# Performance work log

Hardware: AMD Instinct MI355X
Metric: run time of the kernel (lower is better)

The kernel has to match this reference:

```python
import jax, jax.numpy as jnp
import numpy as np

B, N, D, H = 1, 2048, 2048, 16
K = D // H  # head dim = 128


def setup_inputs() -> dict:
    key = jax.random.key(0)
    k1, k2, k3 = jax.random.split(key, 3)
    x = jax.random.normal(k1, (B, N, D), dtype=jnp.float32)
    # torch Linear(D, 3D, bias=False): y = x @ W.T; we store the transposed weight directly.
    W_qkv = jax.random.normal(k2, (D, 3 * D), dtype=jnp.float32) * 0.02
    W_out = jax.random.normal(k3, (D, D), dtype=jnp.float32) * 0.02
    return {"x": x, "W_qkv": W_qkv, "W_out": W_out}


def reference(x, W_qkv, W_out):
    b, n, d = x.shape
    qkv = (x @ W_qkv).reshape(b, n, 3, H, K)  # [B,N,3,H,K]
    q, k, v = qkv[:, :, 0], qkv[:, :, 1], qkv[:, :, 2]  # each [B,N,H,K]
    scale = np.float32(1.0 / np.sqrt(K))
    scores = jnp.einsum('bnhk,bmhk->bnhm', q, k) * scale  # [B,N,H,M]
    causal_mask = jnp.tril(jnp.ones((n, n), dtype=bool))  # [N,M]
    scores = jnp.where(causal_mask[None, :, None, :], scores, jnp.float32(-jnp.inf))
    probs = jax.nn.softmax(scores, axis=-1)
    attn = jnp.einsum('bnhm,bmhk->bnhk', probs, v).reshape(b, n, d)
    return attn @ W_out
```

## Files before the change

### kernel.cpp

```cpp
#include <hip/hip_runtime.h>
#include <hip/hip_bf16.h>
#include <math.h>

#define N_SEQ  2048
#define DMODEL 2048
#define NHEAD  16
#define HDIM   128
#define QKV_LD 6144

typedef __attribute__((ext_vector_type(8))) short bf16x8;
typedef __attribute__((ext_vector_type(4))) float f32x4;

__device__ __forceinline__ ushort f2bf(float x) {
    union { float f; unsigned u; } v; v.f = x;
    unsigned r = (v.u + 0x7fffu + ((v.u >> 16) & 1u)) >> 16;
    return (ushort)r;
}
__device__ __forceinline__ float bf2f(ushort h) {
    union { unsigned u; float f; } v; v.u = ((unsigned)h) << 16;
    return v.f;
}

__global__ __launch_bounds__(256)
void convert_split(const float* __restrict__ in, ushort* __restrict__ oh,
                   ushort* __restrict__ ol, int n4)
{
    int i = blockIdx.x * 256 + threadIdx.x;
    if (i >= n4) return;
    float4 v = ((const float4*)in)[i];
    ushort4 h, l;
    h.x = f2bf(v.x); l.x = f2bf(v.x - bf2f(h.x));
    h.y = f2bf(v.y); l.y = f2bf(v.y - bf2f(h.y));
    h.z = f2bf(v.z); l.z = f2bf(v.z - bf2f(h.z));
    h.w = f2bf(v.w); l.w = f2bf(v.w - bf2f(h.w));
    ((ushort4*)oh)[i] = h;
    ((ushort4*)ol)[i] = l;
}

__global__ __launch_bounds__(256)
void convert_split_t(const float* __restrict__ in, ushort* __restrict__ oh,
                     ushort* __restrict__ ol, int R, int C)
{
    __shared__ float T[64][65];
    const int t = threadIdx.x;
    const int c0 = blockIdx.x * 64, r0 = blockIdx.y * 64;
    #pragma unroll
    for (int p = 0; p < 4; ++p) {
        int r = (t >> 4) + p * 16;
        int c4 = (t & 15) * 4;
        float4 v = *(const float4*)&in[(size_t)(r0 + r) * C + c0 + c4];
        T[r][c4] = v.x; T[r][c4 + 1] = v.y; T[r][c4 + 2] = v.z; T[r][c4 + 3] = v.w;
    }
    __syncthreads();
    #pragma unroll
    for (int p = 0; p < 4; ++p) {
        int c = (t >> 4) + p * 16;
        int r4 = (t & 15) * 4;
        float f0 = T[r4][c], f1 = T[r4 + 1][c], f2 = T[r4 + 2][c], f3 = T[r4 + 3][c];
        ushort4 h, l;
        h.x = f2bf(f0); l.x = f2bf(f0 - bf2f(h.x));
        h.y = f2bf(f1); l.y = f2bf(f1 - bf2f(h.y));
        h.z = f2bf(f2); l.z = f2bf(f2 - bf2f(h.z));
        h.w = f2bf(f3); l.w = f2bf(f3 - bf2f(h.w));
        *(ushort4*)&oh[(size_t)(c0 + c) * R + r0 + r4] = h;
        *(ushort4*)&ol[(size_t)(c0 + c) * R + r0 + r4] = l;
    }
}

__global__ __launch_bounds__(256)
void transpose_v(const ushort* __restrict__ qkvh, ushort* __restrict__ vt)
{
    __shared__ ushort T[64][72];
    const int t = threadIdx.x;
    const int c0 = blockIdx.x * 64, n0 = blockIdx.y * 64;
    #pragma unroll
    for (int p = 0; p < 2; ++p) {
        int r = (t >> 3) + p * 32;
        int u = (t & 7) * 8;
        *(bf16x8*)&T[r][u] = *(const bf16x8*)&qkvh[(size_t)(n0 + r) * QKV_LD + 2 * DMODEL + c0 + u];
    }
    __syncthreads();
    #pragma unroll
    for (int p = 0; p < 2; ++p) {
        int d = (t >> 3) + p * 32;
        int ju = (t & 7) * 8;
        bf16x8 o;
        #pragma unroll
        for (int i = 0; i < 8; ++i) o[i] = (short)T[ju + i][d];
        *(bf16x8*)&vt[(size_t)(c0 + d) * N_SEQ + n0 + ju] = o;
    }
}

#define GBM 256
#define GBN 256
#define GBK 32
#define GPITCH 68

template<bool BF16OUT>
__global__ __launch_bounds__(512, 2)
void gemm_bf16x3_v2(const ushort* __restrict__ Ah_g, const ushort* __restrict__ Al_g,
                    const ushort* __restrict__ Bh_g, const ushort* __restrict__ Bl_g,
                    ushort* __restrict__ Ch, ushort* __restrict__ Cl,
                    float* __restrict__ Cf, int M, int N, int K)
{
    __shared__ ushort bufA[2][GBM * GPITCH];
    __shared__ ushort bufB[2][GBN * GPITCH];

    const int t = threadIdx.x;
    const int l = t & 63;
    const int w = t >> 6;
    const int l15 = l & 15, kgr = l >> 4;
    const int wm = (w >> 2) * 128;
    const int wn = (w & 3) * 64;

    const int nbx = N / GBN, nby = M / GBM;
    const int nwg = nbx * nby;
    int flat = blockIdx.x + blockIdx.y * nbx;
    if ((nwg & 7) == 0) flat = (flat & 7) * (nwg >> 3) + (flat >> 3);
    const int bm = (flat / nbx) * GBM;
    const int bn = (flat % nbx) * GBN;

    const int rA = t >> 1;
    const int hA = t & 1;
    const ushort* gA = (hA ? Al_g : Ah_g) + (size_t)(bm + rA) * K;
    const ushort* gB = (hA ? Bl_g : Bh_g) + (size_t)(bn + rA) * K;

    bf16x8 stA[4], stB[4];
    auto load_regs = [&](int k0) {
        #pragma unroll
        for (int j = 0; j < 4; ++j) {
            stA[j] = *(const bf16x8*)(gA + k0 + j * 8);
            stB[j] = *(const bf16x8*)(gB + k0 + j * 8);
        }
    };
    auto write_lds = [&](int b) {
        #pragma unroll
        for (int j = 0; j < 4; ++j) {
            *(bf16x8*)&bufA[b][rA * GPITCH + hA * 32 + j * 8] = stA[j];
            *(bf16x8*)&bufB[b][rA * GPITCH + hA * 32 + j * 8] = stB[j];
        }
    };

    f32x4 acc[8][4] = {};

    const int nt = K / GBK;
    load_regs(0);
    write_lds(0);
    load_regs(GBK);

    for (int i = 0; i < nt; ++i) {
        const int c = i & 1;
        asm volatile("s_waitcnt lgkmcnt(0)\n\ts_barrier" ::: "memory");
        if (i + 1 < nt) write_lds(c ^ 1);
        if (i + 2 < nt) load_regs((i + 2) * GBK);

        bf16x8 bh[4], bl[4];
        #pragma unroll
        for (int nf = 0; nf < 4; ++nf) {
            const int r = wn + nf * 16 + l15;
            bh[nf] = *(const bf16x8*)&bufB[c][r * GPITCH + kgr * 8];
            bl[nf] = *(const bf16x8*)&bufB[c][r * GPITCH + 32 + kgr * 8];
        }
        #pragma unroll
        for (int mf = 0; mf < 8; ++mf) {
            const int r = wm + mf * 16 + l15;
            bf16x8 ah = *(const bf16x8*)&bufA[c][r * GPITCH + kgr * 8];
            bf16x8 al = *(const bf16x8*)&bufA[c][r * GPITCH + 32 + kgr * 8];
            #pragma unroll
            for (int nf = 0; nf < 4; ++nf) {
                acc[mf][nf] = __builtin_amdgcn_mfma_f32_16x16x32_bf16(ah, bh[nf], acc[mf][nf], 0, 0, 0);
                acc[mf][nf] = __builtin_amdgcn_mfma_f32_16x16x32_bf16(ah, bl[nf], acc[mf][nf], 0, 0, 0);
                acc[mf][nf] = __builtin_amdgcn_mfma_f32_16x16x32_bf16(al, bh[nf], acc[mf][nf], 0, 0, 0);
            }
        }
    }

    #pragma unroll
    for (int mf = 0; mf < 8; ++mf)
        #pragma unroll
        for (int nf = 0; nf < 4; ++nf)
            #pragma unroll
            for (int r = 0; r < 4; ++r) {
                const int m = bm + wm + mf * 16 + kgr * 4 + r;
                const int n = bn + wn + nf * 16 + l15;
                const float v = acc[mf][nf][r];
                if constexpr (BF16OUT) {
                    ushort h = f2bf(v);
                    Ch[(size_t)m * N + n] = h;
                    Cl[(size_t)m * N + n] = f2bf(v - bf2f(h));
                } else {
                    Cf[(size_t)m * N + n] = v;
                }
            }
}

template<bool BF16OUT>
__global__ __launch_bounds__(256, 2)
void gemm_bf16x3(const ushort* __restrict__ Ah_g, const ushort* __restrict__ Al_g,
                 const ushort* __restrict__ Bh_g, const ushort* __restrict__ Bl_g,
                 ushort* __restrict__ Ch, ushort* __restrict__ Cl,
                 float* __restrict__ Cf, int M, int N, int K)
{
    __shared__ ushort Ah[128 * 40], Al[128 * 40], Bh[128 * 40], Bl[128 * 40];
    const int t = threadIdx.x;
    const int l = t & 63;
    const int w = t >> 6;
    const int l15 = l & 15, kgr = l >> 4;
    const int wm = (w >> 1) * 64, wn = (w & 1) * 64;
    const int bm = blockIdx.y * 128, bn = blockIdx.x * 128;
    const int sr = t >> 2, sku = (t & 3) * 8;

    f32x4 acc[4][4] = {};
    bf16x8 sA[4], sB[4];

    auto load_stage = [&](int k0) {
        const size_t a0 = (size_t)(bm + sr) * K + k0 + sku;
        const size_t a1 = (size_t)(bm + sr + 64) * K + k0 + sku;
        sA[0] = *(const bf16x8*)(Ah_g + a0);
        sA[1] = *(const bf16x8*)(Ah_g + a1);
        sA[2] = *(const bf16x8*)(Al_g + a0);
        sA[3] = *(const bf16x8*)(Al_g + a1);
        const size_t b0 = (size_t)(bn + sr) * K + k0 + sku;
        const size_t b1 = (size_t)(bn + sr + 64) * K + k0 + sku;
        sB[0] = *(const bf16x8*)(Bh_g + b0);
        sB[1] = *(const bf16x8*)(Bh_g + b1);
        sB[2] = *(const bf16x8*)(Bl_g + b0);
        sB[3] = *(const bf16x8*)(Bl_g + b1);
    };
    auto write_stage = [&]() {
        *(bf16x8*)&Ah[sr * 40 + sku]        = sA[0];
        *(bf16x8*)&Ah[(sr + 64) * 40 + sku] = sA[1];
        *(bf16x8*)&Al[sr * 40 + sku]        = sA[2];
        *(bf16x8*)&Al[(sr + 64) * 40 + sku] = sA[3];
        *(bf16x8*)&Bh[sr * 40 + sku]        = sB[0];
        *(bf16x8*)&Bh[(sr + 64) * 40 + sku] = sB[1];
        *(bf16x8*)&Bl[sr * 40 + sku]        = sB[2];
        *(bf16x8*)&Bl[(sr + 64) * 40 + sku] = sB[3];
    };

    load_stage(0);
    for (int k0 = 0; k0 < K; k0 += 32) {
        __syncthreads();
        write_stage();
        __syncthreads();
        if (k0 + 32 < K) load_stage(k0 + 32);

        bf16x8 ah[4], al[4], bh[4], bl[4];
        #pragma unroll
        for (int mf = 0; mf < 4; ++mf) {
            ah[mf] = *(const bf16x8*)&Ah[(wm + mf * 16 + l15) * 40 + kgr * 8];
            al[mf] = *(const bf16x8*)&Al[(wm + mf * 16 + l15) * 40 + kgr * 8];
        }
        #pragma unroll
        for (int nf = 0; nf < 4; ++nf) {
            bh[nf] = *(const bf16x8*)&Bh[(wn + nf * 16 + l15) * 40 + kgr * 8];
            bl[nf] = *(const bf16x8*)&Bl[(wn + nf * 16 + l15) * 40 + kgr * 8];
        }
        #pragma unroll
        for (int mf = 0; mf < 4; ++mf)
            #pragma unroll
            for (int nf = 0; nf < 4; ++nf) {
                acc[mf][nf] = __builtin_amdgcn_mfma_f32_16x16x32_bf16(ah[mf], bh[nf], acc[mf][nf], 0, 0, 0);
                acc[mf][nf] = __builtin_amdgcn_mfma_f32_16x16x32_bf16(ah[mf], bl[nf], acc[mf][nf], 0, 0, 0);
                acc[mf][nf] = __builtin_amdgcn_mfma_f32_16x16x32_bf16(al[mf], bh[nf], acc[mf][nf], 0, 0, 0);
            }
    }

    #pragma unroll
    for (int mf = 0; mf < 4; ++mf)
        #pragma unroll
        for (int nf = 0; nf < 4; ++nf)
            #pragma unroll
            for (int r = 0; r < 4; ++r) {
                const int m = bm + wm + mf * 16 + kgr * 4 + r;
                const int n = bn + wn + nf * 16 + l15;
                const float v = acc[mf][nf][r];
                if constexpr (BF16OUT) {
                    ushort h = f2bf(v);
                    Ch[(size_t)m * N + n] = h;
                    Cl[(size_t)m * N + n] = f2bf(v - bf2f(h));
                } else {
                    Cf[(size_t)m * N + n] = v;
                }
            }
}

__global__ __launch_bounds__(256, 2)
void attn_mfma(const ushort* __restrict__ qkvh, const ushort* __restrict__ qkvl,
               const ushort* __restrict__ vt,
               ushort* __restrict__ oh, ushort* __restrict__ ol)
{
    __shared__ ushort Kh[64 * 136], Kl[64 * 136], Vts[128 * 72], St[4 * 16 * 72];
    const int t = threadIdx.x;
    const int l = t & 63;
    const int w = t >> 6;
    const int l15 = l & 15, kgr = l >> 4;
    const int h = blockIdx.y, qb = blockIdx.x;
    const int q0 = qb * 64 + w * 16;

    bf16x8 qh[4], ql[4];
    {
        const size_t base = (size_t)(q0 + l15) * QKV_LD + h * HDIM;
        #pragma unroll
        for (int kc = 0; kc < 4; ++kc) {
            qh[kc] = *(const bf16x8*)(qkvh + base + kc * 32 + kgr * 8);
            ql[kc] = *(const bf16x8*)(qkvl + base + kc * 32 + kgr * 8);
        }
    }

    f32x4 o[8] = {};
    float m_run[4], l_run[4];
    #pragma unroll
    for (int r = 0; r < 4; ++r) { m_run[r] = -1e30f; l_run[r] = 0.f; }

    bf16x8 sKh[4], sKl[4], sV[4];
    auto load_tile = [&](int jb) {
        #pragma unroll
        for (int i = 0; i < 4; ++i) {
            int r = (t >> 4) + i * 16;
            size_t g = (size_t)(jb + r) * QKV_LD + DMODEL + h * HDIM + (t & 15) * 8;
            sKh[i] = *(const bf16x8*)(qkvh + g);
            sKl[i] = *(const bf16x8*)(qkvl + g);
        }
        #pragma unroll
        for (int i = 0; i < 4; ++i) {
            int d = (t >> 3) + i * 32;
            sV[i] = *(const bf16x8*)(vt + (size_t)(h * HDIM + d) * N_SEQ + jb + (t & 7) * 8);
        }
    };
    auto write_tile = [&]() {
        #pragma unroll
        for (int i = 0; i < 4; ++i) {
            int r = (t >> 4) + i * 16;
            *(bf16x8*)&Kh[r * 136 + (t & 15) * 8] = sKh[i];
            *(bf16x8*)&Kl[r * 136 + (t & 15) * 8] = sKl[i];
        }
        #pragma unroll
        for (int i = 0; i < 4; ++i) {
            int d = (t >> 3) + i * 32;
            *(bf16x8*)&Vts[d * 72 + (t & 7) * 8] = sV[i];
        }
    };

    const float scale = 0.08838834764831845f;

    load_tile(0);
    for (int jt = 0; jt <= qb; ++jt) {
        const int jb = jt * 64;
        __syncthreads();
        write_tile();
        __syncthreads();
        if (jt < qb) load_tile(jb + 64);

        float sv[4][4];
        #pragma unroll
        for (int jf = 0; jf < 4; ++jf) {
            f32x4 sacc = {};
            #pragma unroll
            for (int kc = 0; kc < 4; ++kc) {
                bf16x8 kh = *(const bf16x8*)&Kh[(jf * 16 + l15) * 136 + kc * 32 + kgr * 8];
                bf16x8 kl = *(const bf16x8*)&Kl[(jf * 16 + l15) * 136 + kc * 32 + kgr * 8];
                sacc = __builtin_amdgcn_mfma_f32_16x16x32_bf16(qh[kc], kh, sacc, 0, 0, 0);
                sacc = __builtin_amdgcn_mfma_f32_16x16x32_bf16(qh[kc], kl, sacc, 0, 0, 0);
                sacc = __builtin_amdgcn_mfma_f32_16x16x32_bf16(ql[kc], kh, sacc, 0, 0, 0);
            }
            const int j = jb + jf * 16 + l15;
            #pragma unroll
            for (int r = 0; r < 4; ++r) {
                const int q = q0 + kgr * 4 + r;
                sv[jf][r] = (j > q) ? -1e30f : sacc[r] * scale;
            }
        }

        float corr[4], p[4][4];
        #pragma unroll
        for (int r = 0; r < 4; ++r) {
            float tm = fmaxf(fmaxf(sv[0][r], sv[1][r]), fmaxf(sv[2][r], sv[3][r]));
            tm = fmaxf(tm, __shfl_xor(tm, 1));
            tm = fmaxf(tm, __shfl_xor(tm, 2));
            tm = fmaxf(tm, __shfl_xor(tm, 4));
            tm = fmaxf(tm, __shfl_xor(tm, 8));
            const float nm = fmaxf(m_run[r], tm);
            corr[r] = __expf(m_run[r] - nm);
            m_run[r] = nm;
            float rs = 0.f;
            #pragma unroll
            for (int jf = 0; jf < 4; ++jf) { p[jf][r] = __expf(sv[jf][r] - nm); rs += p[jf][r]; }
            rs += __shfl_xor(rs, 1);
            rs += __shfl_xor(rs, 2);
            rs += __shfl_xor(rs, 4);
            rs += __shfl_xor(rs, 8);
            l_run[r] = l_run[r] * corr[r] + rs;
        }

        #pragma unroll
        for (int jf = 0; jf < 4; ++jf)
            #pragma unroll
            for (int r = 0; r < 4; ++r)
                St[w * 1152 + (kgr * 4 + r) * 72 + jf * 16 + l15] = f2bf(p[jf][r]);

        #pragma unroll
        for (int df = 0; df < 8; ++df)
            #pragma unroll
            for (int r = 0; r < 4; ++r) o[df][r] *= corr[r];

        #pragma unroll
        for (int jc = 0; jc < 2; ++jc) {
            bf16x8 pa = *(const bf16x8*)&St[w * 1152 + l15 * 72 + jc * 32 + kgr * 8];
            #pragma unroll
            for (int df = 0; df < 8; ++df) {
                bf16x8 vb = *(const bf16x8*)&Vts[(df * 16 + l15) * 72 + jc * 32 + kgr * 8];
                o[df] = __builtin_amdgcn_mfma_f32_16x16x32_bf16(pa, vb, o[df], 0, 0, 0);
            }
        }
    }

    #pragma unroll
    for (int r = 0; r < 4; ++r) l_run[r] = 1.f / l_run[r];
    #pragma unroll
    for (int df = 0; df < 8; ++df)
        #pragma unroll
        for (int r = 0; r < 4; ++r) {
            const float v = o[df][r] * l_run[r];
            const size_t a = (size_t)(q0 + kgr * 4 + r) * DMODEL + h * HDIM + df * 16 + l15;
            const ushort hh = f2bf(v);
            oh[a] = hh;
            ol[a] = f2bf(v - bf2f(hh));
        }
}

extern "C" void kernel_launch(void* const* d_in, const int* in_sizes, int n_in,
                              void* d_out, int out_size, void* d_ws, size_t ws_size,
                              hipStream_t stream)
{
    const float* x    = (const float*)d_in[0];
    const float* Wqkv = (const float*)d_in[1];
    const float* Wout = (const float*)d_in[2];
    float* outp = (float*)d_out;

    const size_t O_XHI = 0;
    const size_t O_XLO = 8388608;
    const size_t O_WT  = 16777216;
    const size_t O_QKV = 67108864;

    char* ws = (char*)d_ws;
    ushort* x_hi   = (ushort*)(ws + O_XHI);
    ushort* x_lo   = (ushort*)(ws + O_XLO);
    ushort* wqt_hi = (ushort*)(ws + O_WT);
    ushort* wqt_lo = (ushort*)(ws + O_WT + 25165824);
    ushort* qkv_hi = (ushort*)(ws + O_QKV);
    ushort* qkv_lo = (ushort*)(ws + O_QKV + 25165824);
    ushort* wot_hi = (ushort*)(ws + O_WT);
    ushort* wot_lo = (ushort*)(ws + O_WT + 8388608);
    ushort* vt     = (ushort*)(ws + O_WT + 16777216);
    ushort* at_hi  = (ushort*)(ws + O_XHI);
    ushort* at_lo  = (ushort*)(ws + O_XLO);

    convert_split<<<dim3(N_SEQ * DMODEL / 4 / 256), 256, 0, stream>>>(
        x, x_hi, x_lo, N_SEQ * DMODEL / 4);
    convert_split_t<<<dim3(QKV_LD / 64, DMODEL / 64), 256, 0, stream>>>(
        Wqkv, wqt_hi, wqt_lo, DMODEL, QKV_LD);
    gemm_bf16x3_v2<true><<<dim3(QKV_LD / GBN, N_SEQ / GBM), 512, 0, stream>>>(
        x_hi, x_lo, wqt_hi, wqt_lo, qkv_hi, qkv_lo, nullptr,
        N_SEQ, QKV_LD, DMODEL);
    convert_split_t<<<dim3(DMODEL / 64, DMODEL / 64), 256, 0, stream>>>(
        Wout, wot_hi, wot_lo, DMODEL, DMODEL);
    transpose_v<<<dim3(DMODEL / 64, N_SEQ / 64), 256, 0, stream>>>(qkv_hi, vt);
    attn_mfma<<<dim3(N_SEQ / 64, NHEAD), 256, 0, stream>>>(
        qkv_hi, qkv_lo, vt, at_hi, at_lo);
    gemm_bf16x3<false><<<dim3(DMODEL / 128, N_SEQ / 128), 256, 0, stream>>>(
        at_hi, at_lo, wot_hi, wot_lo, nullptr, nullptr, outp,
        N_SEQ, DMODEL, DMODEL);
}
```

Measured before the change: 519.3 us.

## Shrink QKV GEMM tile, pair causal query blocks in attention, unify GEMMs

The QKV projection GEMM moves from 256x256 tiles with 512 threads to 128x128 tiles with 256 threads, giving more workgroups across the CUs. The same double-buffered kernel now also handles the output projection, replacing the older single-buffered GEMM. Attention gives each workgroup two query blocks, b and 31-b, so the causal work per block is even. It also double-buffers the K/V tiles with lighter barriers. The cost is more registers for the two sets of Q fragments and accumulators, which may lower occupancy.

```diff
diff --git a/kernel.cpp b/kernel.cpp
--- a/kernel.cpp
+++ b/kernel.cpp
@@ -91,34 +91,27 @@
     }
 }
 
-#define GBM 256
-#define GBN 256
-#define GBK 32
-#define GPITCH 68
-
 template<bool BF16OUT>
-__global__ __launch_bounds__(512, 2)
-void gemm_bf16x3_v2(const ushort* __restrict__ Ah_g, const ushort* __restrict__ Al_g,
+__global__ __launch_bounds__(256, 2)
+void gemm_bf16x3_v3(const ushort* __restrict__ Ah_g, const ushort* __restrict__ Al_g,
                     const ushort* __restrict__ Bh_g, const ushort* __restrict__ Bl_g,
                     ushort* __restrict__ Ch, ushort* __restrict__ Cl,
                     float* __restrict__ Cf, int M, int N, int K)
 {
-    __shared__ ushort bufA[2][GBM * GPITCH];
-    __shared__ ushort bufB[2][GBN * GPITCH];
+    __shared__ ushort bufA[2][128 * 68];
+    __shared__ ushort bufB[2][128 * 68];
 
     const int t = threadIdx.x;
-    const int l = t & 63;
-    const int w = t >> 6;
+    const int l = t & 63, w = t >> 6;
     const int l15 = l & 15, kgr = l >> 4;
-    const int wm = (w >> 2) * 128;
-    const int wn = (w & 3) * 64;
-
-    const int nbx = N / GBN, nby = M / GBM;
-    const int nwg = nbx * nby;
+    const int wm = (w >> 1) * 64, wn = (w & 1) * 64;
+
+    const int nbx = N / 128;
+    const int nwg = nbx * (M / 128);
     int flat = blockIdx.x + blockIdx.y * nbx;
     if ((nwg & 7) == 0) flat = (flat & 7) * (nwg >> 3) + (flat >> 3);
-    const int bm = (flat / nbx) * GBM;
-    const int bn = (flat % nbx) * GBN;
+    const int bm = (flat / nbx) * 128;
+    const int bn = (flat % nbx) * 128;
 
     const int rA = t >> 1;
     const int hA = t & 1;
@@ -133,39 +126,38 @@
             stB[j] = *(const bf16x8*)(gB + k0 + j * 8);
         }
     };
-    auto write_lds = [&](int b) {
+    auto write_lds = [&](int bsel) {
         #pragma unroll
         for (int j = 0; j < 4; ++j) {
-            *(bf16x8*)&bufA[b][rA * GPITCH + hA * 32 + j * 8] = stA[j];
-            *(bf16x8*)&bufB[b][rA * GPITCH + hA * 32 + j * 8] = stB[j];
+            *(bf16x8*)&bufA[bsel][rA * 68 + hA * 32 + j * 8] = stA[j];
+            *(bf16x8*)&bufB[bsel][rA * 68 + hA * 32 + j * 8] = stB[j];
         }
     };
 
-    f32x4 acc[8][4] = {};
-
-    const int nt = K / GBK;
+    f32x4 acc[4][4] = {};
+    const int nt = K / 32;
     load_regs(0);
     write_lds(0);
-    load_regs(GBK);
+    load_regs(32);
 
     for (int i = 0; i < nt; ++i) {
         const int c = i & 1;
         asm volatile("s_waitcnt lgkmcnt(0)\n\ts_barrier" ::: "memory");
         if (i + 1 < nt) write_lds(c ^ 1);
-        if (i + 2 < nt) load_regs((i + 2) * GBK);
+        if (i + 2 < nt) load_regs((i + 2) * 32);
 
         bf16x8 bh[4], bl[4];
         #pragma unroll
         for (int nf = 0; nf < 4; ++nf) {
             const int r = wn + nf * 16 + l15;
-            bh[nf] = *(const bf16x8*)&bufB[c][r * GPITCH + kgr * 8];
-            bl[nf] = *(const bf16x8*)&bufB[c][r * GPITCH + 32 + kgr * 8];
-        }
-        #pragma unroll
-        for (int mf = 0; mf < 8; ++mf) {
+            bh[nf] = *(const bf16x8*)&bufB[c][r * 68 + kgr * 8];
+            bl[nf] = *(const bf16x8*)&bufB[c][r * 68 + 32 + kgr * 8];
+        }
+        #pragma unroll
+        for (int mf = 0; mf < 4; ++mf) {
             const int r = wm + mf * 16 + l15;
-            bf16x8 ah = *(const bf16x8*)&bufA[c][r * GPITCH + kgr * 8];
-            bf16x8 al = *(const bf16x8*)&bufA[c][r * GPITCH + 32 + kgr * 8];
+            bf16x8 ah = *(const bf16x8*)&bufA[c][r * 68 + kgr * 8];
+            bf16x8 al = *(const bf16x8*)&bufA[c][r * 68 + 32 + kgr * 8];
             #pragma unroll
             for (int nf = 0; nf < 4; ++nf) {
                 acc[mf][nf] = __builtin_amdgcn_mfma_f32_16x16x32_bf16(ah, bh[nf], acc[mf][nf], 0, 0, 0);
@@ -176,7 +168,7 @@
     }
 
     #pragma unroll
-    for (int mf = 0; mf < 8; ++mf)
+    for (int mf = 0; mf < 4; ++mf)
         #pragma unroll
         for (int nf = 0; nf < 4; ++nf)
             #pragma unroll
@@ -194,124 +186,41 @@
             }
 }
 
-template<bool BF16OUT>
-__global__ __launch_bounds__(256, 2)
-void gemm_bf16x3(const ushort* __restrict__ Ah_g, const ushort* __restrict__ Al_g,
-                 const ushort* __restrict__ Bh_g, const ushort* __restrict__ Bl_g,
-                 ushort* __restrict__ Ch, ushort* __restrict__ Cl,
-                 float* __restrict__ Cf, int M, int N, int K)
-{
-    __shared__ ushort Ah[128 * 40], Al[128 * 40], Bh[128 * 40], Bl[128 * 40];
+__global__ __launch_bounds__(256)
+void attn_mfma2(const ushort* __restrict__ qkvh, const ushort* __restrict__ qkvl,
+                const ushort* __restrict__ vt,
+                ushort* __restrict__ oh, ushort* __restrict__ ol)
+{
+    __shared__ ushort Kh[2][64 * 136], Kl[2][64 * 136];
+    __shared__ ushort Vts[2][128 * 68];
+    __shared__ ushort St[4][32 * 68];
+
     const int t = threadIdx.x;
     const int l = t & 63;
     const int w = t >> 6;
     const int l15 = l & 15, kgr = l >> 4;
-    const int wm = (w >> 1) * 64, wn = (w & 1) * 64;
-    const int bm = blockIdx.y * 128, bn = blockIdx.x * 128;
-    const int sr = t >> 2, sku = (t & 3) * 8;
-
-    f32x4 acc[4][4] = {};
-    bf16x8 sA[4], sB[4];
-
-    auto load_stage = [&](int k0) {
-        const size_t a0 = (size_t)(bm + sr) * K + k0 + sku;
-        const size_t a1 = (size_t)(bm + sr + 64) * K + k0 + sku;
-        sA[0] = *(const bf16x8*)(Ah_g + a0);
-        sA[1] = *(const bf16x8*)(Ah_g + a1);
-        sA[2] = *(const bf16x8*)(Al_g + a0);
-        sA[3] = *(const bf16x8*)(Al_g + a1);
-        const size_t b0 = (size_t)(bn + sr) * K + k0 + sku;
-        const size_t b1 = (size_t)(bn + sr + 64) * K + k0 + sku;
-        sB[0] = *(const bf16x8*)(Bh_g + b0);
-        sB[1] = *(const bf16x8*)(Bh_g + b1);
-        sB[2] = *(const bf16x8*)(Bl_g + b0);
-        sB[3] = *(const bf16x8*)(Bl_g + b1);
-    };
-    auto write_stage = [&]() {
-        *(bf16x8*)&Ah[sr * 40 + sku]        = sA[0];
-        *(bf16x8*)&Ah[(sr + 64) * 40 + sku] = sA[1];
-        *(bf16x8*)&Al[sr * 40 + sku]        = sA[2];
-        *(bf16x8*)&Al[(sr + 64) * 40 + sku] = sA[3];
-        *(bf16x8*)&Bh[sr * 40 + sku]        = sB[0];
-        *(bf16x8*)&Bh[(sr + 64) * 40 + sku] = sB[1];
-        *(bf16x8*)&Bl[sr * 40 + sku]        = sB[2];
-        *(bf16x8*)&Bl[(sr + 64) * 40 + sku] = sB[3];
-    };
-
-    load_stage(0);
-    for (int k0 = 0; k0 < K; k0 += 32) {
-        __syncthreads();
-        write_stage();
-        __syncthreads();
-        if (k0 + 32 < K) load_stage(k0 + 32);
-
-        bf16x8 ah[4], al[4], bh[4], bl[4];
-        #pragma unroll
-        for (int mf = 0; mf < 4; ++mf) {
-            ah[mf] = *(const bf16x8*)&Ah[(wm + mf * 16 + l15) * 40 + kgr * 8];
-            al[mf] = *(const bf16x8*)&Al[(wm + mf * 16 + l15) * 40 + kgr * 8];
-        }
-        #pragma unroll
-        for (int nf = 0; nf < 4; ++nf) {
-            bh[nf] = *(const bf16x8*)&Bh[(wn + nf * 16 + l15) * 40 + kgr * 8];
-            bl[nf] = *(const bf16x8*)&Bl[(wn + nf * 16 + l15) * 40 + kgr * 8];
-        }
-        #pragma unroll
-        for (int mf = 0; mf < 4; ++mf)
-            #pragma unroll
-            for (int nf = 0; nf < 4; ++nf) {
-                acc[mf][nf] = __builtin_amdgcn_mfma_f32_16x16x32_bf16(ah[mf], bh[nf], acc[mf][nf], 0, 0, 0);
-                acc[mf][nf] = __builtin_amdgcn_mfma_f32_16x16x32_bf16(ah[mf], bl[nf], acc[mf][nf], 0, 0, 0);
-                acc[mf][nf] = __builtin_amdgcn_mfma_f32_16x16x32_bf16(al[mf], bh[nf], acc[mf][nf], 0, 0, 0);
-            }
-    }
-
-    #pragma unroll
-    for (int mf = 0; mf < 4; ++mf)
-        #pragma unroll
-        for (int nf = 0; nf < 4; ++nf)
-            #pragma unroll
-            for (int r = 0; r < 4; ++r) {
-                const int m = bm + wm + mf * 16 + kgr * 4 + r;
-                const int n = bn + wn + nf * 16 + l15;
-                const float v = acc[mf][nf][r];
-                if constexpr (BF16OUT) {
-                    ushort h = f2bf(v);
-                    Ch[(size_t)m * N + n] = h;
-                    Cl[(size_t)m * N + n] = f2bf(v - bf2f(h));
-                } else {
-                    Cf[(size_t)m * N + n] = v;
-                }
-            }
-}
-
-__global__ __launch_bounds__(256, 2)
-void attn_mfma(const ushort* __restrict__ qkvh, const ushort* __restrict__ qkvl,
-               const ushort* __restrict__ vt,
-               ushort* __restrict__ oh, ushort* __restrict__ ol)
-{
-    __shared__ ushort Kh[64 * 136], Kl[64 * 136], Vts[128 * 72], St[4 * 16 * 72];
-    const int t = threadIdx.x;
-    const int l = t & 63;
-    const int w = t >> 6;
-    const int l15 = l & 15, kgr = l >> 4;
-    const int h = blockIdx.y, qb = blockIdx.x;
-    const int q0 = qb * 64 + w * 16;
-
-    bf16x8 qh[4], ql[4];
-    {
-        const size_t base = (size_t)(q0 + l15) * QKV_LD + h * HDIM;
+    const int h = blockIdx.y, b = blockIdx.x;
+    const int q00 = b * 64 + w * 16;
+    const int q01 = (31 - b) * 64 + w * 16;
+    const int ntiles = 32 - b;
+
+    bf16x8 qh[2][4], ql[2][4];
+    #pragma unroll
+    for (int f = 0; f < 2; ++f) {
+        const size_t base = (size_t)((f ? q01 : q00) + l15) * QKV_LD + h * HDIM;
         #pragma unroll
         for (int kc = 0; kc < 4; ++kc) {
-            qh[kc] = *(const bf16x8*)(qkvh + base + kc * 32 + kgr * 8);
-            ql[kc] = *(const bf16x8*)(qkvl + base + kc * 32 + kgr * 8);
-        }
-    }
-
-    f32x4 o[8] = {};
-    float m_run[4], l_run[4];
-    #pragma unroll
-    for (int r = 0; r < 4; ++r) { m_run[r] = -1e30f; l_run[r] = 0.f; }
+            qh[f][kc] = *(const bf16x8*)(qkvh + base + kc * 32 + kgr * 8);
+            ql[f][kc] = *(const bf16x8*)(qkvl + base + kc * 32 + kgr * 8);
+        }
+    }
+
+    f32x4 o[2][8] = {};
+    float m_run[2][4], l_run[2][4];
+    #pragma unroll
+    for (int f = 0; f < 2; ++f)
+        #pragma unroll
+        for (int r = 0; r < 4; ++r) { m_run[f][r] = -1e30f; l_run[f][r] = 0.f; }
 
     bf16x8 sKh[4], sKl[4], sV[4];
     auto load_tile = [&](int jb) {
@@ -328,105 +237,134 @@
             sV[i] = *(const bf16x8*)(vt + (size_t)(h * HDIM + d) * N_SEQ + jb + (t & 7) * 8);
         }
     };
-    auto write_tile = [&]() {
+    auto write_tile = [&](int c) {
         #pragma unroll
         for (int i = 0; i < 4; ++i) {
             int r = (t >> 4) + i * 16;
-            *(bf16x8*)&Kh[r * 136 + (t & 15) * 8] = sKh[i];
-            *(bf16x8*)&Kl[r * 136 + (t & 15) * 8] = sKl[i];
+            *(bf16x8*)&Kh[c][r * 136 + (t & 15) * 8] = sKh[i];
+            *(bf16x8*)&Kl[c][r * 136 + (t & 15) * 8] = sKl[i];
         }
         #pragma unroll
         for (int i = 0; i < 4; ++i) {
             int d = (t >> 3) + i * 32;
-            *(bf16x8*)&Vts[d * 72 + (t & 7) * 8] = sV[i];
+            *(bf16x8*)&Vts[c][d * 68 + (t & 7) * 8] = sV[i];
         }
     };
 
     const float scale = 0.08838834764831845f;
 
     load_tile(0);
-    for (int jt = 0; jt <= qb; ++jt) {
+    write_tile(0);
+    load_tile(64);
+
+    for (int jt = 0; jt < ntiles; ++jt) {
         const int jb = jt * 64;
-        __syncthreads();
-        write_tile();
-        __syncthreads();
-        if (jt < qb) load_tile(jb + 64);
-
-        float sv[4][4];
+        const int c = jt & 1;
+        asm volatile("s_waitcnt lgkmcnt(0)\n\ts_barrier" ::: "memory");
+        if (jt + 1 < ntiles) write_tile(c ^ 1);
+        if (jt + 2 < ntiles) load_tile(jb + 128);
+
+        const bool f0on = (jt <= b);
+
+        float sv[2][4][4];
         #pragma unroll
         for (int jf = 0; jf < 4; ++jf) {
-            f32x4 sacc = {};
+            f32x4 sacc0 = {}, sacc1 = {};
             #pragma unroll
             for (int kc = 0; kc < 4; ++kc) {
-                bf16x8 kh = *(const bf16x8*)&Kh[(jf * 16 + l15) * 136 + kc * 32 + kgr * 8];
-                bf16x8 kl = *(const bf16x8*)&Kl[(jf * 16 + l15) * 136 + kc * 32 + kgr * 8];
-                sacc = __builtin_amdgcn_mfma_f32_16x16x32_bf16(qh[kc], kh, sacc, 0, 0, 0);
-                sacc = __builtin_amdgcn_mfma_f32_16x16x32_bf16(qh[kc], kl, sacc, 0, 0, 0);
-                sacc = __builtin_amdgcn_mfma_f32_16x16x32_bf16(ql[kc], kh, sacc, 0, 0, 0);
+                bf16x8 kh = *(const bf16x8*)&Kh[c][(jf * 16 + l15) * 136 + kc * 32 + kgr * 8];
+                bf16x8 kl = *(const bf16x8*)&Kl[c][(jf * 16 + l15) * 136 + kc * 32 + kgr * 8];
+                sacc1 = __builtin_amdgcn_mfma_f32_16x16x32_bf16(qh[1][kc], kh, sacc1, 0, 0, 0);
+                sacc1 = __builtin_amdgcn_mfma_f32_16x16x32_bf16(qh[1][kc], kl, sacc1, 0, 0, 0);
+                sacc1 = __builtin_amdgcn_mfma_f32_16x16x32_bf16(ql[1][kc], kh, sacc1, 0, 0, 0);
+                if (f0on) {
+                    sacc0 = __builtin_amdgcn_mfma_f32_16x16x32_bf16(qh[0][kc], kh, sacc0, 0, 0, 0);
+                    sacc0 = __builtin_amdgcn_mfma_f32_16x16x32_bf16(qh[0][kc], kl, sacc0, 0, 0, 0);
+                    sacc0 = __builtin_amdgcn_mfma_f32_16x16x32_bf16(ql[0][kc], kh, sacc0, 0, 0, 0);
+                }
             }
             const int j = jb + jf * 16 + l15;
             #pragma unroll
             for (int r = 0; r < 4; ++r) {
-                const int q = q0 + kgr * 4 + r;
-                sv[jf][r] = (j > q) ? -1e30f : sacc[r] * scale;
-            }
-        }
-
-        float corr[4], p[4][4];
-        #pragma unroll
-        for (int r = 0; r < 4; ++r) {
-            float tm = fmaxf(fmaxf(sv[0][r], sv[1][r]), fmaxf(sv[2][r], sv[3][r]));
-            tm = fmaxf(tm, __shfl_xor(tm, 1));
-            tm = fmaxf(tm, __shfl_xor(tm, 2));
-            tm = fmaxf(tm, __shfl_xor(tm, 4));
-            tm = fmaxf(tm, __shfl_xor(tm, 8));
-            const float nm = fmaxf(m_run[r], tm);
-            corr[r] = __expf(m_run[r] - nm);
-            m_run[r] = nm;
-            float rs = 0.f;
-            #pragma unroll
-            for (int jf = 0; jf < 4; ++jf) { p[jf][r] = __expf(sv[jf][r] - nm); rs += p[jf][r]; }
-            rs += __shfl_xor(rs, 1);
-            rs += __shfl_xor(rs, 2);
-            rs += __shfl_xor(rs, 4);
-            rs += __shfl_xor(rs, 8);
-            l_run[r] = l_run[r] * corr[r] + rs;
-        }
-
-        #pragma unroll
-        for (int jf = 0; jf < 4; ++jf)
-            #pragma unroll
-            for (int r = 0; r < 4; ++r)
-                St[w * 1152 + (kgr * 4 + r) * 72 + jf * 16 + l15] = f2bf(p[jf][r]);
-
+                sv[1][jf][r] = (j > q01 + kgr * 4 + r) ? -1e30f : sacc1[r] * scale;
+                if (f0on)
+                    sv[0][jf][r] = (j > q00 + kgr * 4 + r) ? -1e30f : sacc0[r] * scale;
+            }
+        }
+
+        float corr[2][4];
+        #pragma unroll
+        for (int f = 0; f < 2; ++f) {
+            if (f == 0 && !f0on) continue;
+            #pragma unroll
+            for (int r = 0; r < 4; ++r) {
+                float tm = fmaxf(fmaxf(sv[f][0][r], sv[f][1][r]),
+                                 fmaxf(sv[f][2][r], sv[f][3][r]));
+                tm = fmaxf(tm, __shfl_xor(tm, 1));
+                tm = fmaxf(tm, __shfl_xor(tm, 2));
+                tm = fmaxf(tm, __shfl_xor(tm, 4));
+                tm = fmaxf(tm, __shfl_xor(tm, 8));
+                const float nm = fmaxf(m_run[f][r], tm);
+                corr[f][r] = __expf(m_run[f][r] - nm);
+                m_run[f][r] = nm;
+                float rs = 0.f;
+                const int row = f * 16 + kgr * 4 + r;
+                #pragma unroll
+                for (int jf = 0; jf < 4; ++jf) {
+                    const float pv = __expf(sv[f][jf][r] - nm);
+                    St[w][row * 68 + jf * 16 + l15] = f2bf(pv);
+                    rs += pv;
+                }
+                rs += __shfl_xor(rs, 1);
+                rs += __shfl_xor(rs, 2);
+                rs += __shfl_xor(rs, 4);
+                rs += __shfl_xor(rs, 8);
+                l_run[f][r] = l_run[f][r] * corr[f][r] + rs;
+            }
+        }
+
+        #pragma unroll
+        for (int f = 0; f < 2; ++f) {
+            if (f == 0 && !f0on) continue;
+            #pragma unroll
+            for (int df = 0; df < 8; ++df)
+                #pragma unroll
+                for (int r = 0; r < 4; ++r) o[f][df][r] *= corr[f][r];
+        }
+
+        #pragma unroll
+        for (int jc = 0; jc < 2; ++jc) {
+            bf16x8 pa1 = *(const bf16x8*)&St[w][(16 + l15) * 68 + jc * 32 + kgr * 8];
+            bf16x8 pa0 = {};
+            if (f0on) pa0 = *(const bf16x8*)&St[w][l15 * 68 + jc * 32 + kgr * 8];
+            #pragma unroll
+            for (int df = 0; df < 8; ++df) {
+                bf16x8 vb = *(const bf16x8*)&Vts[c][(df * 16 + l15) * 68 + jc * 32 + kgr * 8];
+                o[1][df] = __builtin_amdgcn_mfma_f32_16x16x32_bf16(pa1, vb, o[1][df], 0, 0, 0);
+                if (f0on)
+                    o[0][df] = __builtin_amdgcn_mfma_f32_16x16x32_bf16(pa0, vb, o[0][df], 0, 0, 0);
+            }
+        }
+    }
+
+    #pragma unroll
+    for (int f = 0; f < 2; ++f)
+        #pragma unroll
+        for (int r = 0; r < 4; ++r) l_run[f][r] = 1.f / l_run[f][r];
+    #pragma unroll
+    for (int f = 0; f < 2; ++f) {
+        const int q0 = f ? q01 : q00;
         #pragma unroll
         for (int df = 0; df < 8; ++df)
             #pragma unroll
-            for (int r = 0; r < 4; ++r) o[df][r] *= corr[r];
-
-        #pragma unroll
-        for (int jc = 0; jc < 2; ++jc) {
-            bf16x8 pa = *(const bf16x8*)&St[w * 1152 + l15 * 72 + jc * 32 + kgr * 8];
-            #pragma unroll
-            for (int df = 0; df < 8; ++df) {
-                bf16x8 vb = *(const bf16x8*)&Vts[(df * 16 + l15) * 72 + jc * 32 + kgr * 8];
-                o[df] = __builtin_amdgcn_mfma_f32_16x16x32_bf16(pa, vb, o[df], 0, 0, 0);
-            }
-        }
-    }
-
-    #pragma unroll
-    for (int r = 0; r < 4; ++r) l_run[r] = 1.f / l_run[r];
-    #pragma unroll
-    for (int df = 0; df < 8; ++df)
-        #pragma unroll
-        for (int r = 0; r < 4; ++r) {
-            const float v = o[df][r] * l_run[r];
-            const size_t a = (size_t)(q0 + kgr * 4 + r) * DMODEL + h * HDIM + df * 16 + l15;
-            const ushort hh = f2bf(v);
-            oh[a] = hh;
-            ol[a] = f2bf(v - bf2f(hh));
-        }
+            for (int r = 0; r < 4; ++r) {
+                const float v = o[f][df][r] * l_run[f][r];
+                const size_t a = (size_t)(q0 + kgr * 4 + r) * DMODEL + h * HDIM + df * 16 + l15;
+                const ushort hh = f2bf(v);
+                oh[a] = hh;
+                ol[a] = f2bf(v - bf2f(hh));
+            }
+    }
 }
 
 extern "C" void kernel_launch(void* const* d_in, const int* in_sizes, int n_in,
@@ -460,15 +398,15 @@
         x, x_hi, x_lo, N_SEQ * DMODEL / 4);
     convert_split_t<<<dim3(QKV_LD / 64, DMODEL / 64), 256, 0, stream>>>(
         Wqkv, wqt_hi, wqt_lo, DMODEL, QKV_LD);
-    gemm_bf16x3_v2<true><<<dim3(QKV_LD / GBN, N_SEQ / GBM), 512, 0, stream>>>(
+    gemm_bf16x3_v3<true><<<dim3(QKV_LD / 128, N_SEQ / 128), 256, 0, stream>>>(
         x_hi, x_lo, wqt_hi, wqt_lo, qkv_hi, qkv_lo, nullptr,
         N_SEQ, QKV_LD, DMODEL);
     convert_split_t<<<dim3(DMODEL / 64, DMODEL / 64), 256, 0, stream>>>(
         Wout, wot_hi, wot_lo, DMODEL, DMODEL);
     transpose_v<<<dim3(DMODEL / 64, N_SEQ / 64), 256, 0, stream>>>(qkv_hi, vt);
-    attn_mfma<<<dim3(N_SEQ / 64, NHEAD), 256, 0, stream>>>(
+    attn_mfma2<<<dim3(16, NHEAD), 256, 0, stream>>>(
         qkv_hi, qkv_lo, vt, at_hi, at_lo);
-    gemm_bf16x3<false><<<dim3(DMODEL / 128, N_SEQ / 128), 256, 0, stream>>>(
+    gemm_bf16x3_v3<false><<<dim3(DMODEL / 128, N_SEQ / 128), 256, 0, stream>>>(
         at_hi, at_lo, wot_hi, wot_lo, nullptr, nullptr, outp,
         N_SEQ, DMODEL, DMODEL);
 }
```

After: 561.2 us. 8.1% more time.
